# Optimization experiments

Measured on AMD Instinct MI355X. Metric: run time of the kernel, lower is better.

## Reference

```python
import jax, jax.numpy as jnp
import numpy as np

B, N, K = 4, 8192, 16
D_POINTS, D_MODEL, INIT_DIM = 64, 64, 3

def _lin(key, din, dout, bias=True):
    k1, k2 = jax.random.split(key)
    s = 1.0 / np.sqrt(din)
    w = jax.random.uniform(k1, (din, dout), minval=-s, maxval=s, dtype=jnp.float32)
    if not bias:
        return w
    b = jax.random.uniform(k2, (dout,), minval=-s, maxval=s, dtype=jnp.float32)
    return w, b

def setup_inputs() -> dict:
    key = jax.random.key(0)
    ks = jax.random.split(key, 12)
    xyz = jax.random.normal(ks[0], (B, N, INIT_DIM), dtype=jnp.float32)
    features = jax.random.normal(ks[1], (B, N, D_POINTS), dtype=jnp.float32)
    knn_idx = jax.random.randint(ks[2], (B, N, K), 0, N)
    fc1_w, fc1_b = _lin(ks[3], D_POINTS, D_MODEL)
    fc2_w, fc2_b = _lin(ks[4], D_MODEL, D_POINTS)
    d1_w, d1_b = _lin(ks[5], INIT_DIM, D_MODEL)
    d2_w, d2_b = _lin(ks[6], D_MODEL, D_MODEL)
    g1_w, g1_b = _lin(ks[7], D_MODEL, D_MODEL)
    g2_w, g2_b = _lin(ks[8], D_MODEL, D_MODEL)
    wq = _lin(ks[9], D_MODEL, D_MODEL, bias=False)
    wk = _lin(ks[10], D_MODEL, D_MODEL, bias=False)
    wv = _lin(ks[11], D_MODEL, D_MODEL, bias=False)
    return dict(xyz=xyz, features=features, knn_idx=knn_idx,
                fc1_w=fc1_w, fc1_b=fc1_b, fc2_w=fc2_w, fc2_b=fc2_b,
                d1_w=d1_w, d1_b=d1_b, d2_w=d2_w, d2_b=d2_b,
                g1_w=g1_w, g1_b=g1_b, g2_w=g2_w, g2_b=g2_b,
                wq=wq, wk=wk, wv=wv)

def _index_points(x, idx):
    # x: (B, N, D), idx: (B, M, K) -> (B, M, K, D)
    return jax.vmap(lambda xb, ib: xb[ib])(x, idx)

def reference(xyz, features, knn_idx,
              fc1_w, fc1_b, fc2_w, fc2_b,
              d1_w, d1_b, d2_w, d2_b,
              g1_w, g1_b, g2_w, g2_b,
              wq, wk, wv):
    idx = knn_idx[:, :, :K]
    knn_xyz = _index_points(xyz, idx)                      # (B,N,K,3)
    pre = features
    x = features @ fc1_w + fc1_b                           # (B,N,d_model)
    q = x @ wq                                             # (B,N,d_model)
    k = _index_points(x @ wk, idx)                         # (B,N,K,d_model)
    v = _index_points(x @ wv, idx)                         # (B,N,K,d_model)
    rel = xyz[:, :, None, :] - knn_xyz                     # (B,N,K,3)
    pos_enc = jax.nn.relu(rel @ d1_w + d1_b) @ d2_w + d2_b # (B,N,K,d_model)
    h = q[:, :, None, :] - k + pos_enc
    attn = jax.nn.relu(h @ g1_w + g1_b) @ g2_w + g2_b      # (B,N,K,d_model)
    attn = jax.nn.softmax(attn / np.sqrt(D_MODEL), axis=-2)
    res = jnp.einsum('bmnf,bmnf->bmf', attn, v + pos_enc)  # (B,N,d_model)
    res = res @ fc2_w + fc2_b + pre                        # (B,N,d_points)
    return res, attn
```

## Files before the change

### kernel.cpp

```cpp
#include <hip/hip_runtime.h>
#include <hip/hip_bf16.h>

#define B_    4
#define N_    8192
#define TOT   (B_*N_)
#define KNN_  16
#define PPW   8
#define PITCH 80

typedef _Float16 half8  __attribute__((ext_vector_type(8)));
typedef float    floatx4 __attribute__((ext_vector_type(4)));

#define MFMA16(A, Bv, C) __builtin_amdgcn_mfma_f32_16x16x32_f16((A), (Bv), (C), 0, 0, 0)

__device__ __forceinline__ void lds_fence(){
  asm volatile("s_waitcnt lgkmcnt(0)" ::: "memory");
}
__device__ __forceinline__ half8 h8_load_f32(const float* __restrict__ p){
  float4 a = *(const float4*)p;
  float4 b = *(const float4*)(p + 4);
  half8 r;
  r[0] = (_Float16)a.x; r[1] = (_Float16)a.y; r[2] = (_Float16)a.z; r[3] = (_Float16)a.w;
  r[4] = (_Float16)b.x; r[5] = (_Float16)b.y; r[6] = (_Float16)b.z; r[7] = (_Float16)b.w;
  return r;
}

__device__ void fill_w64(half8* dst, const float* __restrict__ W, int tid){
  for (int i = tid; i < 512; i += 256){
    int lane = i & 63, nt = (i >> 6) & 3, kt = i >> 8;
    int n  = nt*16 + (lane & 15);
    int kb = kt*32 + ((lane >> 4) & 3)*8;
    half8 v;
    #pragma unroll
    for (int j = 0; j < 8; j++) v[j] = (_Float16)W[(kb + j)*64 + n];
    dst[i] = v;
  }
}

__global__ __launch_bounds__(256, 3) void k1_qkv(
    const float* __restrict__ feat, const float* __restrict__ fc1w, const float* __restrict__ fc1b,
    const float* __restrict__ wqw, const float* __restrict__ wkw, const float* __restrict__ wvw,
    _Float16* __restrict__ qws, _Float16* __restrict__ kws, _Float16* __restrict__ vws)
{
  __shared__ half8 Sfc1[512], Sq[512], Sk[512], Sv[512];
  __shared__ alignas(16) _Float16 xt[4][16*PITCH];
  const int tid = threadIdx.x;
  fill_w64(Sfc1, fc1w, tid);
  fill_w64(Sq, wqw, tid);
  fill_w64(Sk, wkw, tid);
  fill_w64(Sv, wvw, tid);
  __syncthreads();

  const int wave = tid >> 6, lane = tid & 63, quad = lane >> 4, m16 = lane & 15;
  _Float16* tx = &xt[wave][0];
  const int rowbase = blockIdx.x*64 + wave*16;
  float fb[4];
  #pragma unroll
  for (int nt = 0; nt < 4; nt++) fb[nt] = fc1b[nt*16 + m16];

  const int arow = rowbase + m16;
  half8 Fa0 = h8_load_f32(&feat[arow*64 + quad*8]);
  half8 Fa1 = h8_load_f32(&feat[arow*64 + 32 + quad*8]);
  const floatx4 z4 = {0.f, 0.f, 0.f, 0.f};

  #pragma unroll
  for (int nt = 0; nt < 4; nt++){
    floatx4 acc = MFMA16(Fa0, Sfc1[nt*64 + lane], z4);
    acc = MFMA16(Fa1, Sfc1[(4 + nt)*64 + lane], acc);
    const int col = nt*16 + m16;
    #pragma unroll
    for (int r = 0; r < 4; r++)
      tx[(quad*4 + r)*PITCH + col] = (_Float16)(acc[r] + fb[nt]);
  }
  lds_fence();
  const half8 Ax0 = *(const half8*)&tx[m16*PITCH + quad*8];
  const half8 Ax1 = *(const half8*)&tx[m16*PITCH + 32 + quad*8];

#define EMIT_QKV(S, OUT)                                                      \
  { _Pragma("unroll")                                                         \
    for (int nt = 0; nt < 4; nt++){                                           \
      floatx4 acc = MFMA16(Ax0, S[nt*64 + lane], z4);                         \
      acc = MFMA16(Ax1, S[(4 + nt)*64 + lane], acc);                          \
      _Pragma("unroll")                                                       \
      for (int r = 0; r < 4; r++)                                             \
        OUT[(rowbase + quad*4 + r)*64 + nt*16 + m16] = (_Float16)acc[r];      \
    } }
  EMIT_QKV(Sq, qws)
  EMIT_QKV(Sk, kws)
  EMIT_QKV(Sv, vws)
#undef EMIT_QKV
}

__global__ __launch_bounds__(256, 3) void k2_point(
    const float* __restrict__ xyz, const int* __restrict__ knn,
    const float* __restrict__ d1w, const float* __restrict__ d1b,
    const float* __restrict__ d2w, const float* __restrict__ d2b,
    const float* __restrict__ g1w, const float* __restrict__ g1b,
    const float* __restrict__ g2w, const float* __restrict__ g2b,
    const _Float16* __restrict__ qws, const _Float16* __restrict__ kws,
    const _Float16* __restrict__ vws,
    _Float16* __restrict__ r0, float* __restrict__ attn_out)
{
  __shared__ half8 Sd2[512], Sg1[512], Sg2[512];
  __shared__ float4 Td1[64];
  __shared__ alignas(16) _Float16 tiles[4][2][16*PITCH];
  const int tid = threadIdx.x;
  fill_w64(Sd2, d2w, tid);
  fill_w64(Sg1, g1w, tid);
  fill_w64(Sg2, g2w, tid);
  if (tid < 64)
    Td1[tid] = make_float4(d1w[tid], d1w[64 + tid], d1w[128 + tid], d1b[tid]);
  __syncthreads();

  const int wave = tid >> 6, lane = tid & 63, quad = lane >> 4, m16 = lane & 15;
  _Float16* tA = &tiles[wave][0][0];
  _Float16* tB = &tiles[wave][1][0];

  half8 Fd2[2][4], Fg1[2][4], Fg2[2][4];
  #pragma unroll
  for (int nt = 0; nt < 4; nt++){
    #pragma unroll
    for (int kt = 0; kt < 2; kt++){
      Fd2[kt][nt] = Sd2[(kt*4 + nt)*64 + lane];
      Fg1[kt][nt] = Sg1[(kt*4 + nt)*64 + lane];
      Fg2[kt][nt] = Sg2[(kt*4 + nt)*64 + lane];
    }
  }
  float bd2[4], bg1[4], bg2[4];
  #pragma unroll
  for (int nt = 0; nt < 4; nt++){
    const int c = nt*16 + m16;
    bd2[nt] = d2b[c]; bg1[nt] = g1b[c]; bg2[nt] = g2b[c];
  }
  const floatx4 z4 = {0.f, 0.f, 0.f, 0.f};
  const int wsw = quad << 3;
  const int swz = (quad ^ (m16 >> 2)) << 3;

  const int gpt0 = blockIdx.x*(4*PPW) + wave*PPW;
  const int b    = gpt0 >> 13;
  int grow_n = b*N_ + knn[gpt0*KNN_ + m16];

  for (int p = 0; p < PPW; p++){
    const int gpt  = gpt0 + p;
    const int grow = grow_n;

    const half8 Ka0 = *(const half8*)&kws[grow*64 + quad*8];
    const half8 Ka1 = *(const half8*)&kws[grow*64 + 32 + quad*8];
    const half8 Qa0 = *(const half8*)&qws[gpt*64 + quad*8];
    const half8 Qa1 = *(const half8*)&qws[gpt*64 + 32 + quad*8];
    const float dx = xyz[gpt*3 + 0] - xyz[grow*3 + 0];
    const float dy = xyz[gpt*3 + 1] - xyz[grow*3 + 1];
    const float dz = xyz[gpt*3 + 2] - xyz[grow*3 + 2];

    const int g0 = __shfl(grow, quad*4 + 0);
    const int g1 = __shfl(grow, quad*4 + 1);
    const int g2 = __shfl(grow, quad*4 + 2);
    const int g3 = __shfl(grow, quad*4 + 3);

    if (p < PPW-1) grow_n = b*N_ + knn[(gpt+1)*KNN_ + m16];

    half8 At0, At1;
    #pragma unroll
    for (int j = 0; j < 8; j++){
      const float4 w  = Td1[quad*8 + j];
      const float4 w2 = Td1[32 + quad*8 + j];
      float t  = fmaf(dx, w.x,  fmaf(dy, w.y,  fmaf(dz, w.z,  w.w)));
      float t2 = fmaf(dx, w2.x, fmaf(dy, w2.y, fmaf(dz, w2.z, w2.w)));
      At0[j] = (_Float16)(t  > 0.f ? t  : 0.f);
      At1[j] = (_Float16)(t2 > 0.f ? t2 : 0.f);
    }

    float Pc[4][4];
    #pragma unroll
    for (int nt = 0; nt < 4; nt++){
      floatx4 acc = MFMA16(At0, Fd2[0][nt], z4);
      acc = MFMA16(At1, Fd2[1][nt], acc);
      const int colS = (nt*16 + m16) ^ wsw;
      #pragma unroll
      for (int r = 0; r < 4; r++){
        Pc[nt][r] = acc[r] + bd2[nt];
        tB[(quad*4 + r)*PITCH + colS] = (_Float16)Pc[nt][r];
      }
    }
    lds_fence();
    const half8 Pa0 = *(const half8*)&tB[m16*PITCH + swz];
    const half8 Pa1 = *(const half8*)&tB[m16*PITCH + 32 + swz];
    const half8 H0 = Qa0 - Ka0 + Pa0;
    const half8 H1 = Qa1 - Ka1 + Pa1;

    _Float16 vg0[4], vg1[4], vg2[4], vg3[4];
    #pragma unroll
    for (int nt = 0; nt < 4; nt++){
      const int c = nt*16 + m16;
      vg0[nt] = vws[g0*64 + c];
      vg1[nt] = vws[g1*64 + c];
      vg2[nt] = vws[g2*64 + c];
      vg3[nt] = vws[g3*64 + c];
    }

    #pragma unroll
    for (int nt = 0; nt < 4; nt++){
      floatx4 acc = MFMA16(H0, Fg1[0][nt], z4);
      acc = MFMA16(H1, Fg1[1][nt], acc);
      const int colS = (nt*16 + m16) ^ wsw;
      #pragma unroll
      for (int r = 0; r < 4; r++){
        float t = acc[r] + bg1[nt];
        tA[(quad*4 + r)*PITCH + colS] = (_Float16)(t > 0.f ? t : 0.f);
      }
    }
    lds_fence();
    const half8 U0 = *(const half8*)&tA[m16*PITCH + swz];
    const half8 U1 = *(const half8*)&tA[m16*PITCH + 32 + swz];

    float A2[4][4];
    #pragma unroll
    for (int nt = 0; nt < 4; nt++){
      floatx4 acc = MFMA16(U0, Fg2[0][nt], z4);
      acc = MFMA16(U1, Fg2[1][nt], acc);
      #pragma unroll
      for (int r = 0; r < 4; r++) A2[nt][r] = acc[r] + bg2[nt];
    }

    #pragma unroll
    for (int nt = 0; nt < 4; nt++){
      float mx = fmaxf(fmaxf(A2[nt][0], A2[nt][1]), fmaxf(A2[nt][2], A2[nt][3]));
      mx = fmaxf(mx, __shfl_xor(mx, 16));
      mx = fmaxf(mx, __shfl_xor(mx, 32));
      float s = 0.f;
      #pragma unroll
      for (int r = 0; r < 4; r++){
        float e = exp2f((A2[nt][r] - mx)*0.18033688011112042f);
        A2[nt][r] = e; s += e;
      }
      s += __shfl_xor(s, 16);
      s += __shfl_xor(s, 32);
      const float inv = __builtin_amdgcn_rcpf(s);
      #pragma unroll
      for (int r = 0; r < 4; r++) A2[nt][r] *= inv;
    }

    float* ap = attn_out + (size_t)gpt*(KNN_*64);
    float acc_s[4];
    #pragma unroll
    for (int nt = 0; nt < 4; nt++){
      const int c = nt*16 + m16;
      __builtin_nontemporal_store(A2[nt][0], &ap[(quad*4 + 0)*64 + c]);
      __builtin_nontemporal_store(A2[nt][1], &ap[(quad*4 + 1)*64 + c]);
      __builtin_nontemporal_store(A2[nt][2], &ap[(quad*4 + 2)*64 + c]);
      __builtin_nontemporal_store(A2[nt][3], &ap[(quad*4 + 3)*64 + c]);
      float ssum = A2[nt][0]*((float)vg0[nt] + Pc[nt][0])
                 + A2[nt][1]*((float)vg1[nt] + Pc[nt][1])
                 + A2[nt][2]*((float)vg2[nt] + Pc[nt][2])
                 + A2[nt][3]*((float)vg3[nt] + Pc[nt][3]);
      ssum += __shfl_xor(ssum, 16);
      ssum += __shfl_xor(ssum, 32);
      acc_s[nt] = ssum;
    }
    const float rv = (quad & 2) ? ((quad & 1) ? acc_s[3] : acc_s[2])
                                : ((quad & 1) ? acc_s[1] : acc_s[0]);
    r0[gpt*64 + quad*16 + m16] = (_Float16)rv;
  }
}

__global__ __launch_bounds__(256, 2) void k3_fc2(
    const _Float16* __restrict__ r0, const float* __restrict__ fc2w,
    const float* __restrict__ fc2b, const float* __restrict__ feat,
    float* __restrict__ out_res)
{
  __shared__ half8 S[512];
  const int tid = threadIdx.x;
  fill_w64(S, fc2w, tid);
  __syncthreads();

  const int wave = tid >> 6, lane = tid & 63, quad = lane >> 4, m16 = lane & 15;
  const int rowbase = blockIdx.x*64 + wave*16;
  float fb[4];
  #pragma unroll
  for (int nt = 0; nt < 4; nt++) fb[nt] = fc2b[nt*16 + m16];

  const half8 A0 = *(const half8*)&r0[(rowbase + m16)*64 + quad*8];
  const half8 A1 = *(const half8*)&r0[(rowbase + m16)*64 + 32 + quad*8];
  const floatx4 z4 = {0.f, 0.f, 0.f, 0.f};

  #pragma unroll
  for (int nt = 0; nt < 4; nt++){
    floatx4 acc = MFMA16(A0, S[nt*64 + lane], z4);
    acc = MFMA16(A1, S[(4 + nt)*64 + lane], acc);
    #pragma unroll
    for (int r = 0; r < 4; r++){
      const int rowg = rowbase + quad*4 + r;
      const int col  = nt*16 + m16;
      out_res[rowg*64 + col] = acc[r] + fb[nt] + feat[rowg*64 + col];
    }
  }
}

extern "C" void kernel_launch(void* const* d_in, const int* in_sizes, int n_in,
                              void* d_out, int out_size, void* d_ws, size_t ws_size,
                              hipStream_t stream)
{
  (void)in_sizes; (void)n_in; (void)out_size; (void)ws_size;
  const float* xyz  = (const float*)d_in[0];
  const float* feat = (const float*)d_in[1];
  const int*   knn  = (const int*)d_in[2];
  const float* fc1w = (const float*)d_in[3];
  const float* fc1b = (const float*)d_in[4];
  const float* fc2w = (const float*)d_in[5];
  const float* fc2b = (const float*)d_in[6];
  const float* d1w  = (const float*)d_in[7];
  const float* d1b  = (const float*)d_in[8];
  const float* d2w  = (const float*)d_in[9];
  const float* d2b  = (const float*)d_in[10];
  const float* g1w  = (const float*)d_in[11];
  const float* g1b  = (const float*)d_in[12];
  const float* g2w  = (const float*)d_in[13];
  const float* g2b  = (const float*)d_in[14];
  const float* wq   = (const float*)d_in[15];
  const float* wk   = (const float*)d_in[16];
  const float* wv   = (const float*)d_in[17];

  _Float16* ws  = (_Float16*)d_ws;
  _Float16* qws = ws;
  _Float16* kws = ws + (size_t)TOT*64;
  _Float16* vws = ws + (size_t)2*TOT*64;
  _Float16* r0  = ws + (size_t)3*TOT*64;

  float* out      = (float*)d_out;
  float* out_res  = out;
  float* out_attn = out + (size_t)TOT*64;

  k1_qkv<<<TOT/64, 256, 0, stream>>>(feat, fc1w, fc1b, wq, wk, wv, qws, kws, vws);
  k2_point<<<TOT/(4*PPW), 256, 0, stream>>>(xyz, knn, d1w, d1b, d2w, d2b,
                                            g1w, g1b, g2w, g2b,
                                            qws, kws, vws, r0, out_attn);
  k3_fc2<<<TOT/64, 256, 0, stream>>>(r0, fc2w, fc2b, feat, out_res);
}
```

Before: 307.0 us.

## Raise k2 occupancy, share one LDS tile, prefetch xyz, use plain attn stores

Raises k2_point's launch bound from 3 to 4 blocks per SM and merges the two per-wave LDS transpose tiles into one, cutting shared memory per block. It also moves the xyz loads for the next point and neighbour to the end of the previous iteration so their latency overlaps with other work. The attention output stores switch from nontemporal to ordinary stores. Reusing one tile adds a write-after-read dependency between the two stages, and the tighter register budget may cause spills.

```diff
diff --git a/kernel.cpp b/kernel.cpp
--- a/kernel.cpp
+++ b/kernel.cpp
@@ -91,7 +91,7 @@
 #undef EMIT_QKV
 }
 
-__global__ __launch_bounds__(256, 3) void k2_point(
+__global__ __launch_bounds__(256, 4) void k2_point(
     const float* __restrict__ xyz, const int* __restrict__ knn,
     const float* __restrict__ d1w, const float* __restrict__ d1b,
     const float* __restrict__ d2w, const float* __restrict__ d2b,
@@ -103,7 +103,7 @@
 {
   __shared__ half8 Sd2[512], Sg1[512], Sg2[512];
   __shared__ float4 Td1[64];
-  __shared__ alignas(16) _Float16 tiles[4][2][16*PITCH];
+  __shared__ alignas(16) _Float16 tiles[4][16*PITCH];
   const int tid = threadIdx.x;
   fill_w64(Sd2, d2w, tid);
   fill_w64(Sg1, g1w, tid);
@@ -113,8 +113,7 @@
   __syncthreads();
 
   const int wave = tid >> 6, lane = tid & 63, quad = lane >> 4, m16 = lane & 15;
-  _Float16* tA = &tiles[wave][0][0];
-  _Float16* tB = &tiles[wave][1][0];
+  _Float16* tT = &tiles[wave][0];
 
   half8 Fd2[2][4], Fg1[2][4], Fg2[2][4];
   #pragma unroll
@@ -138,26 +137,29 @@
 
   const int gpt0 = blockIdx.x*(4*PPW) + wave*PPW;
   const int b    = gpt0 >> 13;
-  int grow_n = b*N_ + knn[gpt0*KNN_ + m16];
+
+  int grow_c = b*N_ + knn[gpt0*KNN_ + m16];
+  float xq0 = xyz[gpt0*3 + 0], xq1 = xyz[gpt0*3 + 1], xq2 = xyz[gpt0*3 + 2];
+  float xn0 = xyz[grow_c*3 + 0], xn1 = xyz[grow_c*3 + 1], xn2 = xyz[grow_c*3 + 2];
 
   for (int p = 0; p < PPW; p++){
     const int gpt  = gpt0 + p;
-    const int grow = grow_n;
+    const int grow = grow_c;
 
     const half8 Ka0 = *(const half8*)&kws[grow*64 + quad*8];
     const half8 Ka1 = *(const half8*)&kws[grow*64 + 32 + quad*8];
     const half8 Qa0 = *(const half8*)&qws[gpt*64 + quad*8];
     const half8 Qa1 = *(const half8*)&qws[gpt*64 + 32 + quad*8];
-    const float dx = xyz[gpt*3 + 0] - xyz[grow*3 + 0];
-    const float dy = xyz[gpt*3 + 1] - xyz[grow*3 + 1];
-    const float dz = xyz[gpt*3 + 2] - xyz[grow*3 + 2];
 
     const int g0 = __shfl(grow, quad*4 + 0);
     const int g1 = __shfl(grow, quad*4 + 1);
     const int g2 = __shfl(grow, quad*4 + 2);
     const int g3 = __shfl(grow, quad*4 + 3);
 
+    int grow_n = 0;
     if (p < PPW-1) grow_n = b*N_ + knn[(gpt+1)*KNN_ + m16];
+
+    const float dx = xq0 - xn0, dy = xq1 - xn1, dz = xq2 - xn2;
 
     half8 At0, At1;
     #pragma unroll
@@ -179,12 +181,12 @@
       #pragma unroll
       for (int r = 0; r < 4; r++){
         Pc[nt][r] = acc[r] + bd2[nt];
-        tB[(quad*4 + r)*PITCH + colS] = (_Float16)Pc[nt][r];
+        tT[(quad*4 + r)*PITCH + colS] = (_Float16)Pc[nt][r];
       }
     }
     lds_fence();
-    const half8 Pa0 = *(const half8*)&tB[m16*PITCH + swz];
-    const half8 Pa1 = *(const half8*)&tB[m16*PITCH + 32 + swz];
+    const half8 Pa0 = *(const half8*)&tT[m16*PITCH + swz];
+    const half8 Pa1 = *(const half8*)&tT[m16*PITCH + 32 + swz];
     const half8 H0 = Qa0 - Ka0 + Pa0;
     const half8 H1 = Qa1 - Ka1 + Pa1;
 
@@ -206,12 +208,12 @@
       #pragma unroll
       for (int r = 0; r < 4; r++){
         float t = acc[r] + bg1[nt];
-        tA[(quad*4 + r)*PITCH + colS] = (_Float16)(t > 0.f ? t : 0.f);
+        tT[(quad*4 + r)*PITCH + colS] = (_Float16)(t > 0.f ? t : 0.f);
       }
     }
     lds_fence();
-    const half8 U0 = *(const half8*)&tA[m16*PITCH + swz];
-    const half8 U1 = *(const half8*)&tA[m16*PITCH + 32 + swz];
+    const half8 U0 = *(const half8*)&tT[m16*PITCH + swz];
+    const half8 U1 = *(const half8*)&tT[m16*PITCH + 32 + swz];
 
     float A2[4][4];
     #pragma unroll
@@ -245,10 +247,10 @@
     #pragma unroll
     for (int nt = 0; nt < 4; nt++){
       const int c = nt*16 + m16;
-      __builtin_nontemporal_store(A2[nt][0], &ap[(quad*4 + 0)*64 + c]);
-      __builtin_nontemporal_store(A2[nt][1], &ap[(quad*4 + 1)*64 + c]);
-      __builtin_nontemporal_store(A2[nt][2], &ap[(quad*4 + 2)*64 + c]);
-      __builtin_nontemporal_store(A2[nt][3], &ap[(quad*4 + 3)*64 + c]);
+      ap[(quad*4 + 0)*64 + c] = A2[nt][0];
+      ap[(quad*4 + 1)*64 + c] = A2[nt][1];
+      ap[(quad*4 + 2)*64 + c] = A2[nt][2];
+      ap[(quad*4 + 3)*64 + c] = A2[nt][3];
       float ssum = A2[nt][0]*((float)vg0[nt] + Pc[nt][0])
                  + A2[nt][1]*((float)vg1[nt] + Pc[nt][1])
                  + A2[nt][2]*((float)vg2[nt] + Pc[nt][2])
@@ -260,6 +262,12 @@
     const float rv = (quad & 2) ? ((quad & 1) ? acc_s[3] : acc_s[2])
                                 : ((quad & 1) ? acc_s[1] : acc_s[0]);
     r0[gpt*64 + quad*16 + m16] = (_Float16)rv;
+
+    if (p < PPW-1){
+      grow_c = grow_n;
+      xq0 = xyz[(gpt+1)*3 + 0]; xq1 = xyz[(gpt+1)*3 + 1]; xq2 = xyz[(gpt+1)*3 + 2];
+      xn0 = xyz[grow_n*3 + 0];  xn1 = xyz[grow_n*3 + 1];  xn2 = xyz[grow_n*3 + 2];
+    }
   }
 }
 
```

After: 328.0 us. 6.9% more time.
